# Kernel optimization log

Measured on AMD Instinct MI355X. Metric: run time of the kernel, lower is better.

Reference implementation:

```python
import jax, jax.numpy as jnp
import numpy as np

GRID = 8          # proto_grid
EPS = 1e-4        # safe_norm eps
TAU = 20.0        # temperature used throughout


def avg_pool(x, k):
    # non-overlapping avg pool, kernel k divides H and W exactly
    S, C, H, W = x.shape
    return x.reshape(S, C, H // k, k, W // k, k).mean(axis=(3, 5))


def safe_norm(x, axis):
    n = jnp.sqrt(jnp.sum(x * x, axis=axis, keepdims=True))
    return x / jnp.maximum(n, EPS)


def setup_inputs() -> dict:
    key = jax.random.key(0)
    k1, k2, k3 = jax.random.split(key, 3)
    qry = jax.random.normal(k1, (1, 1, 256, 128, 128), dtype=jnp.float32)
    sup_x = jax.random.normal(k2, (1, 5, 1, 256, 128, 128), dtype=jnp.float32)
    sup_y = jax.random.uniform(k3, (1, 5, 1, 128, 128), dtype=jnp.float32)
    return {"qry": qry, "sup_x": sup_x, "sup_y": sup_y, "thresh": 0}


def reference(qry, sup_x, sup_y, thresh):
    # mode == 'gridconv', use_cross_attn=False, isval=False
    qry = qry[:, 0]          # squeeze(1)        -> [1, 256, 128, 128]
    sup_x = sup_x[0, :, 0]   # squeeze(0,2)      -> [5, 256, 128, 128]
    sup_y = sup_y[0]         # squeeze(0)        -> [5, 1, 128, 128]

    shot, nc, H, W = sup_x.shape
    k = H // GRID

    # grid prototypes: avgpool then [shot, nc, g*g] -> [shot, g*g, nc] -> [shot*g*g, nc]
    n_sup = avg_pool(sup_x, k)
    protos = n_sup.reshape(shot, nc, -1).transpose(0, 2, 1).reshape(-1, nc)
    # selection mask: avg_pool(sup_y) > thresh. sup_y is uniform(0,1) and
    # thresh=0, so every grid cell is selected -> selection is the identity
    # (fixed-shape, jit-safe; matches the torch boolean index exactly here).

    # mean-center then safe L2-normalize (channel dim)
    protos = protos - protos.mean(axis=-1, keepdims=True)
    qryc = qry - qry.mean(axis=1, keepdims=True)
    pro_n = safe_norm(protos, axis=1)        # [npro, nc]
    qry_n = safe_norm(qryc, axis=1)          # [b, nc, h, w]

    # 1x1 conv as cosine similarity against prototype bank
    dists = jnp.einsum('bchw,pc->bphw', qry_n, pro_n) * TAU   # [b, npro, h, w]
    prob = jax.nn.softmax(dists, axis=1)
    # bmm combine: channel-wise weighted prototypes per pixel
    ch_proto = jnp.einsum('pc,bphw->bchw', pro_n, prob)       # [b, nc, h, w]
    pred_grid = jnp.sum(qry_n * ch_proto * TAU, axis=1, keepdims=True)

    debug_assign = jnp.argmax(dists, axis=1).astype(jnp.float32)
    return pred_grid, debug_assign
```

## Files before the change

### kernel.cpp

```cpp
#include <hip/hip_runtime.h>

#define NCH   256
#define NPROT 320
#define HW    16384
#define TAU   20.0f
#define EPSN  1e-4f

typedef _Float16 half8 __attribute__((ext_vector_type(8)));
typedef float    f32x4 __attribute__((ext_vector_type(4)));

__global__ __launch_bounds__(256) void k_pool(const float* __restrict__ sup_x,
                                              float* __restrict__ praw) {
    int b = blockIdx.x;
    int t = threadIdx.x;
    const float4* plane = (const float4*)(sup_x + (size_t)b * HW);
    float rsum[8];
    #pragma unroll
    for (int r = 0; r < 8; ++r) rsum[r] = 0.f;
    #pragma unroll
    for (int i = 0; i < 16; ++i) {
        float4 v = plane[i * 256 + t];
        rsum[i >> 1] += v.x + v.y + v.z + v.w;
    }
    __shared__ float part[8][256];
    #pragma unroll
    for (int r = 0; r < 8; ++r) part[r][t] = rsum[r];
    __syncthreads();
    int R  = t >> 5;
    int cw = t & 31;
    float s = 0.f;
    #pragma unroll
    for (int a = 0; a < 8; ++a) s += part[R][a * 32 + cw];
    s += __shfl_xor(s, 1);
    s += __shfl_xor(s, 2);
    if ((t & 3) == 0) {
        int shot = b >> 8, c = b & 255;
        int p = shot * 64 + R * 8 + (cw >> 2);
        praw[(size_t)p * NCH + c] = s * (1.0f / 256.0f);
    }
}

__device__ __forceinline__ float block_sum256(float x, float* ws4, int t) {
    #pragma unroll
    for (int o = 1; o < 64; o <<= 1) x += __shfl_xor(x, o);
    if ((t & 63) == 0) ws4[t >> 6] = x;
    __syncthreads();
    float r = ws4[0] + ws4[1] + ws4[2] + ws4[3];
    __syncthreads();
    return r;
}

__global__ __launch_bounds__(256) void k_norm(const float* __restrict__ praw,
                                              _Float16* __restrict__ PTh,
                                              _Float16* __restrict__ PTl) {
    int p = blockIdx.x;
    int c = threadIdx.x;
    __shared__ float ws4[4];
    float v = praw[p * NCH + c];
    float mean = block_sum256(v, ws4, c) * (1.0f / 256.0f);
    float cen = v - mean;
    float n2 = block_sum256(cen * cen, ws4, c);
    float inv = 1.0f / fmaxf(sqrtf(n2), EPSN);
    float pn = cen * inv;
    _Float16 hi = (_Float16)pn;
    float lo = (pn - (float)hi) * 2048.0f;
    size_t idx = ((size_t)(c >> 3) * NPROT + p) * 8 + (c & 7);
    PTh[idx] = hi;
    PTl[idx] = (_Float16)lo;
}

__global__ __launch_bounds__(256, 2) void k_main(const float* __restrict__ qry,
                                                 const _Float16* __restrict__ PTh,
                                                 const _Float16* __restrict__ PTl,
                                                 float* __restrict__ out) {
    __shared__ __align__(16) float qlds[32 * 260];
    __shared__ float red1[32 * 33], red2[32 * 33];
    __shared__ __align__(16) _Float16 Ah[32 * 256];
    __shared__ __align__(16) _Float16 Al[32 * 256];
    __shared__ float meanv[32], invnv[32];
    __shared__ float Mw[4][32], Sw[4][32], Tw[4][32], Iw[4][32];
    int t = threadIdx.x;
    int pixbase = blockIdx.x * 32;

    {
        int f4 = t & 7;
        int c0 = t >> 3;
        float ps1[4] = {0.f, 0.f, 0.f, 0.f};
        float ps2[4] = {0.f, 0.f, 0.f, 0.f};
        #pragma unroll
        for (int i = 0; i < 8; ++i) {
            int c = c0 + 32 * i;
            float4 v = *(const float4*)(qry + (size_t)c * HW + pixbase + f4 * 4);
            int px = f4 * 4;
            qlds[(px + 0) * 260 + c] = v.x;
            qlds[(px + 1) * 260 + c] = v.y;
            qlds[(px + 2) * 260 + c] = v.z;
            qlds[(px + 3) * 260 + c] = v.w;
            ps1[0] += v.x; ps2[0] = fmaf(v.x, v.x, ps2[0]);
            ps1[1] += v.y; ps2[1] = fmaf(v.y, v.y, ps2[1]);
            ps1[2] += v.z; ps2[2] = fmaf(v.z, v.z, ps2[2]);
            ps1[3] += v.w; ps2[3] = fmaf(v.w, v.w, ps2[3]);
        }
        #pragma unroll
        for (int j = 0; j < 4; ++j) {
            red1[c0 * 33 + f4 * 4 + j] = ps1[j];
            red2[c0 * 33 + f4 * 4 + j] = ps2[j];
        }
    }
    __syncthreads();
    if (t < 32) {
        float s1 = 0.f, s2 = 0.f;
        #pragma unroll
        for (int j = 0; j < 32; ++j) { s1 += red1[j * 33 + t]; s2 += red2[j * 33 + t]; }
        float mean = s1 * (1.0f / 256.0f);
        float n2 = fmaxf(s2 - s1 * mean, 0.f);
        meanv[t] = mean;
        invnv[t] = 1.0f / fmaxf(sqrtf(n2), EPSN);
    }
    __syncthreads();

    {
        int px = t >> 3, g = t & 7;
        float mean = meanv[px], invn = invnv[px];
        #pragma unroll
        for (int c8 = 0; c8 < 4; ++c8) {
            int k0 = g * 32 + c8 * 8;
            const float* src = &qlds[px * 260 + k0];
            half8 hv, lv;
            #pragma unroll
            for (int j = 0; j < 8; ++j) {
                float qn = (src[j] - mean) * invn;
                _Float16 h = (_Float16)qn;
                hv[j] = h;
                lv[j] = (_Float16)((qn - (float)h) * 2048.0f);
            }
            int off = px * 512 + ((k0 * 2) ^ ((px & 7) << 4));
            *(half8*)((char*)Ah + off) = hv;
            *(half8*)((char*)Al + off) = lv;
        }
    }
    __syncthreads();

    int lane = t & 63, w = t >> 6;
    int col = lane & 15, g4 = lane >> 4;

    f32x4 acc1[2][5], acc2[2][5];
    #pragma unroll
    for (int mt = 0; mt < 2; ++mt)
        #pragma unroll
        for (int nt = 0; nt < 5; ++nt) {
            acc1[mt][nt] = (f32x4){0.f, 0.f, 0.f, 0.f};
            acc2[mt][nt] = (f32x4){0.f, 0.f, 0.f, 0.f};
        }

    {
        const half8* BH = (const half8*)PTh;
        const half8* BL = (const half8*)PTl;
        int nb = w * 80 + col;
        int aswz = (col & 7) << 4;
        const char* AhB = (const char*)Ah + col * 512;
        const char* AlB = (const char*)Al + col * 512;
        #pragma unroll 2
        for (int kb = 0; kb < 8; ++kb) {
            int rowb = (kb * 4 + g4) * 320 + nb;
            half8 bh[5], bl[5];
            #pragma unroll
            for (int nt = 0; nt < 5; ++nt) {
                bh[nt] = BH[rowb + nt * 16];
                bl[nt] = BL[rowb + nt * 16];
            }
            int koff = (kb * 64 + g4 * 16) ^ aswz;
            half8 ah0 = *(const half8*)(AhB + koff);
            half8 ah1 = *(const half8*)(AhB + koff + 8192);
            half8 al0 = *(const half8*)(AlB + koff);
            half8 al1 = *(const half8*)(AlB + koff + 8192);
            #pragma unroll
            for (int nt = 0; nt < 5; ++nt) {
                acc1[0][nt] = __builtin_amdgcn_mfma_f32_16x16x32_f16(ah0, bh[nt], acc1[0][nt], 0, 0, 0);
                acc1[1][nt] = __builtin_amdgcn_mfma_f32_16x16x32_f16(ah1, bh[nt], acc1[1][nt], 0, 0, 0);
                acc2[0][nt] = __builtin_amdgcn_mfma_f32_16x16x32_f16(ah0, bl[nt], acc2[0][nt], 0, 0, 0);
                acc2[0][nt] = __builtin_amdgcn_mfma_f32_16x16x32_f16(al0, bh[nt], acc2[0][nt], 0, 0, 0);
                acc2[1][nt] = __builtin_amdgcn_mfma_f32_16x16x32_f16(ah1, bl[nt], acc2[1][nt], 0, 0, 0);
                acc2[1][nt] = __builtin_amdgcn_mfma_f32_16x16x32_f16(al1, bh[nt], acc2[1][nt], 0, 0, 0);
            }
        }
    }

    #pragma unroll
    for (int mt = 0; mt < 2; ++mt) {
        #pragma unroll
        for (int r = 0; r < 4; ++r) {
            int pixel = mt * 16 + g4 * 4 + r;
            float dv[5];
            #pragma unroll
            for (int nt = 0; nt < 5; ++nt)
                dv[nt] = TAU * (acc1[mt][nt][r] + acc2[mt][nt][r] * (1.0f / 2048.0f));
            float gm = dv[0];
            float gi = (float)(w * 80 + col);
            #pragma unroll
            for (int nt = 1; nt < 5; ++nt)
                if (dv[nt] > gm) { gm = dv[nt]; gi = (float)(w * 80 + nt * 16 + col); }
            #pragma unroll
            for (int o = 1; o < 16; o <<= 1) {
                float om = __shfl_xor(gm, o);
                float oi = __shfl_xor(gi, o);
                if (om > gm || (om == gm && oi < gi)) { gm = om; gi = oi; }
            }
            float S = 0.f, T = 0.f;
            #pragma unroll
            for (int nt = 0; nt < 5; ++nt) {
                float e = __expf(dv[nt] - gm);
                S += e;
                T = fmaf(e, dv[nt], T);
            }
            #pragma unroll
            for (int o = 1; o < 16; o <<= 1) { S += __shfl_xor(S, o); T += __shfl_xor(T, o); }
            if (col == 0) { Mw[w][pixel] = gm; Sw[w][pixel] = S; Tw[w][pixel] = T; Iw[w][pixel] = gi; }
        }
    }
    __syncthreads();

    if (t < 32) {
        float gm = Mw[0][t], gi = Iw[0][t];
        #pragma unroll
        for (int k = 1; k < 4; ++k)
            if (Mw[k][t] > gm) { gm = Mw[k][t]; gi = Iw[k][t]; }
        float S = 0.f, T = 0.f;
        #pragma unroll
        for (int k = 0; k < 4; ++k) {
            float sc = __expf(Mw[k][t] - gm);
            S = fmaf(Sw[k][t], sc, S);
            T = fmaf(Tw[k][t], sc, T);
        }
        out[pixbase + t] = T / S;
        out[HW + pixbase + t] = gi;
    }
}

extern "C" void kernel_launch(void* const* d_in, const int* in_sizes, int n_in,
                              void* d_out, int out_size, void* d_ws, size_t ws_size,
                              hipStream_t stream) {
    const float* qry   = (const float*)d_in[0];
    const float* sup_x = (const float*)d_in[1];
    float* out = (float*)d_out;

    float* praw   = (float*)d_ws;
    _Float16* PTh = (_Float16*)(praw + NPROT * NCH);
    _Float16* PTl = PTh + NPROT * NCH;

    k_pool<<<5 * 256, 256, 0, stream>>>(sup_x, praw);
    k_norm<<<NPROT, 256, 0, stream>>>(praw, PTh, PTl);
    k_main<<<HW / 32, 256, 0, stream>>>(qry, PTh, PTl, out);
}
```

Measured before the change: 159.6 us.

## Fold query centering/normalization into GEMM epilogue, drop fp32 staging buffer

```diff
diff --git a/kernel.cpp b/kernel.cpp
--- a/kernel.cpp
+++ b/kernel.cpp
@@ -52,7 +52,8 @@
 
 __global__ __launch_bounds__(256) void k_norm(const float* __restrict__ praw,
                                               _Float16* __restrict__ PTh,
-                                              _Float16* __restrict__ PTl) {
+                                              _Float16* __restrict__ PTl,
+                                              float* __restrict__ sp) {
     int p = blockIdx.x;
     int c = threadIdx.x;
     __shared__ float ws4[4];
@@ -67,16 +68,18 @@
     size_t idx = ((size_t)(c >> 3) * NPROT + p) * 8 + (c & 7);
     PTh[idx] = hi;
     PTl[idx] = (_Float16)lo;
+    float ssum = block_sum256(pn, ws4, c);
+    if (c == 0) sp[p] = ssum;
 }
 
 __global__ __launch_bounds__(256, 2) void k_main(const float* __restrict__ qry,
                                                  const _Float16* __restrict__ PTh,
                                                  const _Float16* __restrict__ PTl,
+                                                 const float* __restrict__ sp,
                                                  float* __restrict__ out) {
-    __shared__ __align__(16) float qlds[32 * 260];
-    __shared__ float red1[32 * 33], red2[32 * 33];
     __shared__ __align__(16) _Float16 Ah[32 * 256];
     __shared__ __align__(16) _Float16 Al[32 * 256];
+    __shared__ float red1[32 * 33], red2[32 * 33];
     __shared__ float meanv[32], invnv[32];
     __shared__ float Mw[4][32], Sw[4][32], Tw[4][32], Iw[4][32];
     int t = threadIdx.x;
@@ -87,19 +90,25 @@
         int c0 = t >> 3;
         float ps1[4] = {0.f, 0.f, 0.f, 0.f};
         float ps2[4] = {0.f, 0.f, 0.f, 0.f};
+        char* AhB = (char*)Ah;
+        char* AlB = (char*)Al;
         #pragma unroll
         for (int i = 0; i < 8; ++i) {
             int c = c0 + 32 * i;
             float4 v = *(const float4*)(qry + (size_t)c * HW + pixbase + f4 * 4);
-            int px = f4 * 4;
-            qlds[(px + 0) * 260 + c] = v.x;
-            qlds[(px + 1) * 260 + c] = v.y;
-            qlds[(px + 2) * 260 + c] = v.z;
-            qlds[(px + 3) * 260 + c] = v.w;
-            ps1[0] += v.x; ps2[0] = fmaf(v.x, v.x, ps2[0]);
-            ps1[1] += v.y; ps2[1] = fmaf(v.y, v.y, ps2[1]);
-            ps1[2] += v.z; ps2[2] = fmaf(v.z, v.z, ps2[2]);
-            ps1[3] += v.w; ps2[3] = fmaf(v.w, v.w, ps2[3]);
+            float q[4] = {v.x, v.y, v.z, v.w};
+            #pragma unroll
+            for (int j = 0; j < 4; ++j) {
+                int px = f4 * 4 + j;
+                float x = q[j];
+                _Float16 h = (_Float16)x;
+                _Float16 l = (_Float16)((x - (float)h) * 2048.0f);
+                int off = px * 512 + ((2 * c) ^ ((px & 7) << 4));
+                *(_Float16*)(AhB + off) = h;
+                *(_Float16*)(AlB + off) = l;
+                ps1[j] += x;
+                ps2[j] = fmaf(x, x, ps2[j]);
+            }
         }
         #pragma unroll
         for (int j = 0; j < 4; ++j) {
@@ -119,71 +128,50 @@
     }
     __syncthreads();
 
-    {
-        int px = t >> 3, g = t & 7;
-        float mean = meanv[px], invn = invnv[px];
-        #pragma unroll
-        for (int c8 = 0; c8 < 4; ++c8) {
-            int k0 = g * 32 + c8 * 8;
-            const float* src = &qlds[px * 260 + k0];
-            half8 hv, lv;
-            #pragma unroll
-            for (int j = 0; j < 8; ++j) {
-                float qn = (src[j] - mean) * invn;
-                _Float16 h = (_Float16)qn;
-                hv[j] = h;
-                lv[j] = (_Float16)((qn - (float)h) * 2048.0f);
-            }
-            int off = px * 512 + ((k0 * 2) ^ ((px & 7) << 4));
-            *(half8*)((char*)Ah + off) = hv;
-            *(half8*)((char*)Al + off) = lv;
-        }
-    }
-    __syncthreads();
-
     int lane = t & 63, w = t >> 6;
     int col = lane & 15, g4 = lane >> 4;
-
-    f32x4 acc1[2][5], acc2[2][5];
-    #pragma unroll
-    for (int mt = 0; mt < 2; ++mt)
-        #pragma unroll
-        for (int nt = 0; nt < 5; ++nt) {
-            acc1[mt][nt] = (f32x4){0.f, 0.f, 0.f, 0.f};
-            acc2[mt][nt] = (f32x4){0.f, 0.f, 0.f, 0.f};
-        }
-
-    {
-        const half8* BH = (const half8*)PTh;
-        const half8* BL = (const half8*)PTl;
-        int nb = w * 80 + col;
-        int aswz = (col & 7) << 4;
-        const char* AhB = (const char*)Ah + col * 512;
-        const char* AlB = (const char*)Al + col * 512;
+    int aswz = (col & 7) << 4;
+    const char* AhB = (const char*)Ah + col * 512;
+    const char* AlB = (const char*)Al + col * 512;
+    const half8* BH = (const half8*)PTh;
+    const half8* BL = (const half8*)PTl;
+
+    f32x4 dva[2][5];
+    float spv[5];
+
+    #pragma unroll
+    for (int nt = 0; nt < 5; ++nt) {
+        int nb = w * 80 + nt * 16 + col;
+        spv[nt] = sp[nb];
+        f32x4 a1_0 = {0.f, 0.f, 0.f, 0.f}, a1_1 = {0.f, 0.f, 0.f, 0.f};
+        f32x4 a2_0 = {0.f, 0.f, 0.f, 0.f}, a2_1 = {0.f, 0.f, 0.f, 0.f};
+        half8 bh0 = BH[(0 * 4 + g4) * 320 + nb];
+        half8 bl0 = BL[(0 * 4 + g4) * 320 + nb];
+        half8 bh1 = BH[(1 * 4 + g4) * 320 + nb];
+        half8 bl1 = BL[(1 * 4 + g4) * 320 + nb];
         #pragma unroll 2
         for (int kb = 0; kb < 8; ++kb) {
-            int rowb = (kb * 4 + g4) * 320 + nb;
-            half8 bh[5], bl[5];
-            #pragma unroll
-            for (int nt = 0; nt < 5; ++nt) {
-                bh[nt] = BH[rowb + nt * 16];
-                bl[nt] = BL[rowb + nt * 16];
+            half8 bhn{}, bln{};
+            if (kb < 6) {
+                bhn = BH[((kb + 2) * 4 + g4) * 320 + nb];
+                bln = BL[((kb + 2) * 4 + g4) * 320 + nb];
             }
             int koff = (kb * 64 + g4 * 16) ^ aswz;
             half8 ah0 = *(const half8*)(AhB + koff);
             half8 ah1 = *(const half8*)(AhB + koff + 8192);
             half8 al0 = *(const half8*)(AlB + koff);
             half8 al1 = *(const half8*)(AlB + koff + 8192);
-            #pragma unroll
-            for (int nt = 0; nt < 5; ++nt) {
-                acc1[0][nt] = __builtin_amdgcn_mfma_f32_16x16x32_f16(ah0, bh[nt], acc1[0][nt], 0, 0, 0);
-                acc1[1][nt] = __builtin_amdgcn_mfma_f32_16x16x32_f16(ah1, bh[nt], acc1[1][nt], 0, 0, 0);
-                acc2[0][nt] = __builtin_amdgcn_mfma_f32_16x16x32_f16(ah0, bl[nt], acc2[0][nt], 0, 0, 0);
-                acc2[0][nt] = __builtin_amdgcn_mfma_f32_16x16x32_f16(al0, bh[nt], acc2[0][nt], 0, 0, 0);
-                acc2[1][nt] = __builtin_amdgcn_mfma_f32_16x16x32_f16(ah1, bl[nt], acc2[1][nt], 0, 0, 0);
-                acc2[1][nt] = __builtin_amdgcn_mfma_f32_16x16x32_f16(al1, bh[nt], acc2[1][nt], 0, 0, 0);
-            }
-        }
+            a1_0 = __builtin_amdgcn_mfma_f32_16x16x32_f16(ah0, bh0, a1_0, 0, 0, 0);
+            a1_1 = __builtin_amdgcn_mfma_f32_16x16x32_f16(ah1, bh0, a1_1, 0, 0, 0);
+            a2_0 = __builtin_amdgcn_mfma_f32_16x16x32_f16(ah0, bl0, a2_0, 0, 0, 0);
+            a2_0 = __builtin_amdgcn_mfma_f32_16x16x32_f16(al0, bh0, a2_0, 0, 0, 0);
+            a2_1 = __builtin_amdgcn_mfma_f32_16x16x32_f16(ah1, bl0, a2_1, 0, 0, 0);
+            a2_1 = __builtin_amdgcn_mfma_f32_16x16x32_f16(al1, bh0, a2_1, 0, 0, 0);
+            bh0 = bh1; bl0 = bl1;
+            bh1 = bhn; bl1 = bln;
+        }
+        dva[0][nt] = a1_0 + a2_0 * (1.0f / 2048.0f);
+        dva[1][nt] = a1_1 + a2_1 * (1.0f / 2048.0f);
     }
 
     #pragma unroll
@@ -191,10 +179,11 @@
         #pragma unroll
         for (int r = 0; r < 4; ++r) {
             int pixel = mt * 16 + g4 * 4 + r;
+            float mean = meanv[pixel], invn = invnv[pixel];
             float dv[5];
             #pragma unroll
             for (int nt = 0; nt < 5; ++nt)
-                dv[nt] = TAU * (acc1[mt][nt][r] + acc2[mt][nt][r] * (1.0f / 2048.0f));
+                dv[nt] = TAU * invn * (dva[mt][nt][r] - mean * spv[nt]);
             float gm = dv[0];
             float gi = (float)(w * 80 + col);
             #pragma unroll
@@ -247,8 +236,9 @@
     float* praw   = (float*)d_ws;
     _Float16* PTh = (_Float16*)(praw + NPROT * NCH);
     _Float16* PTl = PTh + NPROT * NCH;
+    float* sp     = (float*)(PTl + NPROT * NCH);
 
     k_pool<<<5 * 256, 256, 0, stream>>>(sup_x, praw);
-    k_norm<<<NPROT, 256, 0, stream>>>(praw, PTh, PTl);
-    k_main<<<HW / 32, 256, 0, stream>>>(qry, PTh, PTl, out);
-}
+    k_norm<<<NPROT, 256, 0, stream>>>(praw, PTh, PTl, sp);
+    k_main<<<HW / 32, 256, 0, stream>>>(qry, PTh, PTl, sp, out);
+}
```

After: 160.3 us. About the same (+0.4%).
